# Optimization experiments

Hardware: AMD Instinct MI355X
Metric: run time of the kernel (lower is better)

Reference implementation:

```python
import jax, jax.numpy as jnp
import numpy as np

N_NODES = 20000
N_EDGES = 320000
HIDDEN = 64
HEADS = 8
HEAD_DIM = HIDDEN // HEADS
K_HOPS = 2
CST = 1e-05


def setup_inputs() -> dict:
    key = jax.random.key(0)
    ks = jax.random.split(key, 12)
    s = 1.0 / np.sqrt(HIDDEN)
    inp = {
        "x": jax.random.normal(ks[0], (N_NODES, HIDDEN), dtype=jnp.float32),
        "edge_index": jax.random.randint(ks[1], (2, N_EDGES), 0, N_NODES, dtype=jnp.int64),
        "edge_feature": jnp.zeros((1,), dtype=jnp.float32),  # unused by the module
        "Wq": jax.random.uniform(ks[2], (HIDDEN, HIDDEN), jnp.float32, -s, s),
        "bq": jax.random.uniform(ks[3], (HIDDEN,), jnp.float32, -s, s),
        "Wk": jax.random.uniform(ks[4], (HIDDEN, HIDDEN), jnp.float32, -s, s),
        "bk": jax.random.uniform(ks[5], (HIDDEN,), jnp.float32, -s, s),
        "Wv": jax.random.uniform(ks[6], (HIDDEN, HIDDEN), jnp.float32, -s, s),
        "bv": jax.random.uniform(ks[7], (HIDDEN,), jnp.float32, -s, s),
        "Wo": jax.random.uniform(ks[8], (HIDDEN, HIDDEN), jnp.float32, -s, s),
        "bo": jax.random.uniform(ks[9], (HIDDEN,), jnp.float32, -s, s),
        "hopwise": jnp.ones((K_HOPS + 1,), dtype=jnp.float32),
        "headwise": jnp.zeros((HEADS, K_HOPS), dtype=jnp.float32),
    }
    return inp


def reference(x, edge_index, edge_feature, Wq, bq, Wk, bk, Wv, bv, Wo, bo, hopwise, headwise):
    N = x.shape[0]
    row, col = edge_index[0], edge_index[1]

    # symmetric normalization: deg is in-degree of col
    deg = jax.ops.segment_sum(jnp.ones_like(col, dtype=x.dtype), col, num_segments=N)
    deg_inv = jnp.where(deg > 0, deg ** -0.5, 0.0)
    norm = deg_inv[row] * deg_inv[col]  # [E]

    Q = 1.0 + jax.nn.elu(x @ Wq + bq)
    K = 1.0 + jax.nn.elu(x @ Wk + bk)
    V = (x @ Wv + bv)
    Q = Q.reshape(N, HEADS, HEAD_DIM)
    K = K.reshape(N, HEADS, HEAD_DIM)
    V = V.reshape(N, HEADS, HEAD_DIM)

    M = jnp.einsum('nhi,nhj->nhij', K, V)  # [N,H,d,d]
    hidden = V * hopwise[0]
    layerwise = jax.nn.softmax(headwise, axis=0)  # softmax over heads (dim=-2)

    for hop in range(K_HOPS):
        # scatter-add propagation: out[i] = sum_{e: col[e]=i} norm[e] * state[row[e]]
        M = jax.ops.segment_sum(norm[:, None, None, None] * M[row], col, num_segments=N)
        K = jax.ops.segment_sum(norm[:, None, None] * K[row], col, num_segments=N)
        H = jnp.einsum('nhi,nhij->nhj', Q, M)
        C = jnp.einsum('nhi,nhi->nh', Q, K)[..., None] + CST
        H = H / C
        gamma = hopwise[hop + 1] * layerwise[:, hop][:, None]  # [H,1]
        hidden = hidden + gamma * H

    hidden = hidden.reshape(N, HEADS * HEAD_DIM)
    # dropout is identity in eval mode
    return hidden @ Wo + bo
```

## Files before the change

kernel.cpp:

```cpp
#include <hip/hip_runtime.h>
#include <hip/hip_bf16.h>

typedef __hip_bfloat16 bf16;
typedef __fp16 half2_t __attribute__((ext_vector_type(2)));
typedef float floatx2 __attribute__((ext_vector_type(2)));
typedef _Float16 f16x8_t __attribute__((ext_vector_type(8)));
typedef float f32x4_t __attribute__((ext_vector_type(4)));

#define N_NODES 20000
#define N_EDGES 320000
#define CSTF 1e-5f

#if defined(__has_builtin)
#if __has_builtin(__builtin_amdgcn_cvt_pk_fp8_f32) && __has_builtin(__builtin_amdgcn_cvt_pk_f32_fp8)
#define M1FP8 1
#endif
#if __has_builtin(__builtin_amdgcn_fdot2)
#define HAVE_FDOT2 1
#endif
#endif

#ifdef M1FP8
#define M1_STRIDE 128
#define M1_LANE   2
typedef uint2 m1vec;
#else
#define M1_STRIDE 256
#define M1_LANE   4
typedef uint4 m1vec;
#endif

__device__ __forceinline__ half2_t u2h(unsigned int u) {
    union { unsigned int u; half2_t h; } c; c.u = u; return c.h;
}
__device__ __forceinline__ unsigned int pkh(float a, float b) {
    union { __fp16 h[2]; unsigned int u; } c;
    c.h[0] = (__fp16)a; c.h[1] = (__fp16)b;
    return c.u;
}
__device__ __forceinline__ float fdot2(half2_t a, half2_t b, float c) {
#ifdef HAVE_FDOT2
    return __builtin_amdgcn_fdot2(a, b, c, false);
#else
    return fmaf((float)a.x, (float)b.x, fmaf((float)a.y, (float)b.y, c));
#endif
}
__device__ __forceinline__ int rdl(int v, int lane) { return __builtin_amdgcn_readlane(v, lane); }
__device__ __forceinline__ float ldf(const void* p, int i, bool bf) {
    return bf ? __bfloat162float(((const bf16*)p)[i]) : ((const float*)p)[i];
}
__device__ __forceinline__ bool wave_is_i64(const void* ei, int e) {
    unsigned int hi = ((const unsigned int*)ei)[2 * e + 1];
    return !__any(hi != 0);
}

struct Args {
    const void *x, *ei, *Wq, *bq, *Wk, *bk, *Wv, *bv, *Wo, *bo, *hopwise, *headwise;
    void* out;
    float* Q;
    _Float16 *K0h, *Vh, *K1h;
    unsigned int* M1h;
    int* bsrc;
    float* Hf;
    float* gam;
    int *deg, *cnt;
};

__global__ __launch_bounds__(256) void k_p1(Args a) {
    const int t = threadIdx.x;
    const int e = blockIdx.x * 256 + t;
    bool i64 = wave_is_i64(a.ei, e);
    int r, c;
    if (i64) {
        r = (int)((const long long*)a.ei)[e];
        c = (int)((const long long*)a.ei)[N_EDGES + e];
    } else {
        r = ((const int*)a.ei)[e];
        c = ((const int*)a.ei)[N_EDGES + e];
    }
    int slot = atomicAdd(&a.deg[c], 1);
    if (slot < 64) a.bsrc[c * 64 + slot] = r;
    if (blockIdx.x < 64) {
        int bad = 0;
        for (int i = blockIdx.x * 256 + t; i < 40000; i += 64 * 256) {
            unsigned int w = ((const unsigned int*)a.x)[i];
            if (((w >> 7)  & 0xFFu) == 0xFFu) bad++;
            if (((w >> 23) & 0xFFu) == 0xFFu) bad++;
        }
        if (bad) atomicAdd(&a.cnt[0], bad);
    }
}

__global__ __launch_bounds__(256) void k_qkv(Args a) {
    __shared__ __align__(16) _Float16 sA[4096];
    __shared__ __align__(16) _Float16 sB[12288];
    const int t = threadIdx.x;
    const bool bf = (a.cnt[0] < 16);
    const int n0 = blockIdx.x * 64;

    if (blockIdx.x == 0 && t < 8) {
        float e0 = 0.f, e1 = 0.f;
        for (int hh = 0; hh < 8; hh++) {
            e0 += __expf(ldf(a.headwise, hh * 2 + 0, bf));
            e1 += __expf(ldf(a.headwise, hh * 2 + 1, bf));
        }
        a.gam[t]     = ldf(a.hopwise, 1, bf) * __expf(ldf(a.headwise, t * 2 + 0, bf)) / e0;
        a.gam[8 + t] = ldf(a.hopwise, 2, bf) * __expf(ldf(a.headwise, t * 2 + 1, bf)) / e1;
        if (t == 0) a.gam[16] = ldf(a.hopwise, 0, bf);
    }

    for (int i = t; i < 2048; i += 256) {
        int node = i >> 5, kp = i & 31;
        int gn = n0 + node; if (gn >= N_NODES) gn = N_NODES - 1;
        float x0 = ldf(a.x, gn * 64 + kp * 2 + 0, bf);
        float x1 = ldf(a.x, gn * 64 + kp * 2 + 1, bf);
        int byte = (node * 128 + kp * 4) ^ ((node & 7) << 4);
        *(unsigned int*)((char*)sA + byte) = pkh(x0, x1);
    }
    for (int i = t; i < 6144; i += 256) {
        int kp = i / 192, n = i % 192;
        int k = kp * 2, c = n & 63;
        const void* W = (n < 64) ? a.Wq : (n < 128) ? a.Wk : a.Wv;
        float w0 = ldf(W, k * 64 + c, bf);
        float w1 = ldf(W, (k + 1) * 64 + c, bf);
        int ct = n >> 4, kh = k >> 5, kq = (k & 31) >> 3;
        int hoff = (((ct * 2 + kh) * 64 + kq * 16 + (n & 15)) << 3) + (k & 7);
        *(unsigned int*)&sB[hoff] = pkh(w0, w1);
    }
    __syncthreads();

    const int l = t & 63, w = t >> 6;
    f16x8_t Afrag[2];
    {
        int node = w * 16 + (l & 15);
        int cb = node * 128 + ((l >> 4) * 16);
        int swz = (node & 7) << 4;
        Afrag[0] = *(const f16x8_t*)((const char*)sA + ((cb)      ^ swz));
        Afrag[1] = *(const f16x8_t*)((const char*)sA + ((cb + 64) ^ swz));
    }
    f32x4_t acc[12];
#pragma unroll
    for (int ct = 0; ct < 12; ct++) acc[ct] = (f32x4_t){0.f, 0.f, 0.f, 0.f};
#pragma unroll
    for (int kh = 0; kh < 2; kh++) {
#pragma unroll
        for (int ct = 0; ct < 12; ct++) {
            f16x8_t B = *(const f16x8_t*)&sB[((ct * 2 + kh) * 64 + l) * 8];
            acc[ct] = __builtin_amdgcn_mfma_f32_16x16x32_f16(Afrag[kh], B, acc[ct], 0, 0, 0);
        }
    }
    const int dcol = l & 15;
    float bqv[4], bkv[4], bvv[4];
#pragma unroll
    for (int ct = 0; ct < 4; ct++) {
        bqv[ct] = ldf(a.bq, ct * 16 + dcol, bf);
        bkv[ct] = ldf(a.bk, ct * 16 + dcol, bf);
        bvv[ct] = ldf(a.bv, ct * 16 + dcol, bf);
    }
    const int rbase = n0 + w * 16 + ((l >> 4) << 2);
#pragma unroll
    for (int j = 0; j < 4; j++) {
        int gn = rbase + j;
        if (gn < N_NODES) {
            int dg = a.deg[gn];
            float di = dg > 0 ? rsqrtf((float)dg) : 0.0f;
#pragma unroll
            for (int ct = 0; ct < 4; ct++) {
                float q = acc[ct][j] + bqv[ct];
                a.Q[gn * 64 + ct * 16 + dcol] = q > 0.f ? q + 1.f : __expf(q);
                float kx = acc[4 + ct][j] + bkv[ct];
                float ke = kx > 0.f ? kx + 1.f : __expf(kx);
                a.K0h[gn * 64 + ct * 16 + dcol] = (_Float16)(di * ke);
                a.Vh[gn * 64 + ct * 16 + dcol] = (_Float16)(acc[8 + ct][j] + bvv[ct]);
            }
        }
    }
}

__global__ __launch_bounds__(128) void k_hop1(Args a) {
    const int l = threadIdx.x & 63;
    const int n = blockIdx.x * 2 + (threadIdx.x >> 6);
    const int hb = l & 56;
    float acc[8] = {0, 0, 0, 0, 0, 0, 0, 0};
    float kacc = 0.0f;
    const int dg = a.deg[n];
    const int m = min(dg, 64);
    if (m > 0) {
        const int srcv = a.bsrc[n * 64 + (l < m ? l : m - 1)];
#define H1_BODY(KU, VO, KO)                                                \
    {                                                                      \
        half2_t p0 = u2h(KU.x), p1 = u2h(KU.y), p2 = u2h(KU.z), p3 = u2h(KU.w); \
        float vv = (float)VO;                                              \
        acc[0] = fmaf(vv, (float)p0.x, acc[0]); acc[1] = fmaf(vv, (float)p0.y, acc[1]); \
        acc[2] = fmaf(vv, (float)p1.x, acc[2]); acc[3] = fmaf(vv, (float)p1.y, acc[3]); \
        acc[4] = fmaf(vv, (float)p2.x, acc[4]); acc[5] = fmaf(vv, (float)p2.y, acc[5]); \
        acc[6] = fmaf(vv, (float)p3.x, acc[6]); acc[7] = fmaf(vv, (float)p3.y, acc[7]); \
        kacc += (float)KO;                                                 \
    }
        int e = 0;
        for (; e + 4 <= m; e += 4) {
            int sA = rdl(srcv, e), sB = rdl(srcv, e + 1), sC = rdl(srcv, e + 2), sD = rdl(srcv, e + 3);
            uint4 kA = *(const uint4*)(a.K0h + sA * 64 + hb);
            uint4 kB = *(const uint4*)(a.K0h + sB * 64 + hb);
            uint4 kC = *(const uint4*)(a.K0h + sC * 64 + hb);
            uint4 kD = *(const uint4*)(a.K0h + sD * 64 + hb);
            __fp16 vA = a.Vh[sA * 64 + l], vB = a.Vh[sB * 64 + l];
            __fp16 vC = a.Vh[sC * 64 + l], vD = a.Vh[sD * 64 + l];
            __fp16 oA = a.K0h[sA * 64 + l], oB = a.K0h[sB * 64 + l];
            __fp16 oC = a.K0h[sC * 64 + l], oD = a.K0h[sD * 64 + l];
            H1_BODY(kA, vA, oA)
            H1_BODY(kB, vB, oB)
            H1_BODY(kC, vC, oC)
            H1_BODY(kD, vD, oD)
        }
        for (; e < m; e++) {
            int sA = rdl(srcv, e);
            uint4 kA = *(const uint4*)(a.K0h + sA * 64 + hb);
            __fp16 vA = a.Vh[sA * 64 + l];
            __fp16 oA = a.K0h[sA * 64 + l];
            H1_BODY(kA, vA, oA)
        }
#undef H1_BODY
        float inv = 1.0f / (float)dg;
#pragma unroll
        for (int i = 0; i < 8; i++) acc[i] *= inv;
        kacc *= inv;
    }
#ifdef M1FP8
    unsigned int w0 = 0, w1 = 0;
    w0 = __builtin_amdgcn_cvt_pk_fp8_f32(acc[0], acc[1], w0, false);
    w0 = __builtin_amdgcn_cvt_pk_fp8_f32(acc[2], acc[3], w0, true);
    w1 = __builtin_amdgcn_cvt_pk_fp8_f32(acc[4], acc[5], w1, false);
    w1 = __builtin_amdgcn_cvt_pk_fp8_f32(acc[6], acc[7], w1, true);
    uint2 o2; o2.x = w0; o2.y = w1;
    *(uint2*)(a.M1h + (size_t)n * M1_STRIDE + l * M1_LANE) = o2;
#else
    uint4 o;
    o.x = pkh(acc[0], acc[1]); o.y = pkh(acc[2], acc[3]);
    o.z = pkh(acc[4], acc[5]); o.w = pkh(acc[6], acc[7]);
    *(uint4*)(a.M1h + (size_t)n * M1_STRIDE + l * M1_LANE) = o;
#endif
    a.K1h[n * 64 + l] = (_Float16)kacc;
}

__global__ __launch_bounds__(128) void k_hop2f(Args a) {
    const int l = threadIdx.x & 63;
    const int n = blockIdx.x * 2 + (threadIdx.x >> 6);
    const int hb = l & 56, h = l >> 3;
    const float4 qa = *(const float4*)(a.Q + n * 64 + hb);
    const float4 qb = *(const float4*)(a.Q + n * 64 + hb + 4);
    const float qown = a.Q[n * 64 + l];
    float hacc = 0.0f, sk = 0.0f;
    const int dg = a.deg[n];
    const int m = min(dg, 64);
#ifdef M1FP8
#define H2_DOT(MU, DST)                                                    \
    {                                                                      \
        floatx2 a0 = __builtin_amdgcn_cvt_pk_f32_fp8(MU.x, false);         \
        floatx2 a1 = __builtin_amdgcn_cvt_pk_f32_fp8(MU.x, true);          \
        floatx2 a2 = __builtin_amdgcn_cvt_pk_f32_fp8(MU.y, false);         \
        floatx2 a3 = __builtin_amdgcn_cvt_pk_f32_fp8(MU.y, true);          \
        DST = qa.x * a0.x;                                                 \
        DST = fmaf(qa.y, a0.y, DST); DST = fmaf(qa.z, a1.x, DST);          \
        DST = fmaf(qa.w, a1.y, DST); DST = fmaf(qb.x, a2.x, DST);          \
        DST = fmaf(qb.y, a2.y, DST); DST = fmaf(qb.z, a3.x, DST);          \
        DST = fmaf(qb.w, a3.y, DST);                                       \
    }
#else
    const half2_t q01 = u2h(pkh(qa.x, qa.y));
    const half2_t q23 = u2h(pkh(qa.z, qa.w));
    const half2_t q45 = u2h(pkh(qb.x, qb.y));
    const half2_t q67 = u2h(pkh(qb.z, qb.w));
#define H2_DOT(MU, DST)                                                    \
    {                                                                      \
        DST = fdot2(q01, u2h(MU.x), 0.0f);                                 \
        DST = fdot2(q23, u2h(MU.y), DST);                                  \
        DST = fdot2(q45, u2h(MU.z), DST);                                  \
        DST = fdot2(q67, u2h(MU.w), DST);                                  \
    }
#endif
    if (m > 0) {
        const int srcv = a.bsrc[n * 64 + (l < m ? l : m - 1)];
        int e = 0;
        for (; e + 8 <= m; e += 8) {
            int s_[8];
            m1vec m_[8];
            __fp16 k_[8];
#pragma unroll
            for (int u = 0; u < 8; u++) s_[u] = rdl(srcv, e + u);
#pragma unroll
            for (int u = 0; u < 8; u++) m_[u] = *(const m1vec*)(a.M1h + (size_t)s_[u] * M1_STRIDE + l * M1_LANE);
#pragma unroll
            for (int u = 0; u < 8; u++) k_[u] = a.K1h[s_[u] * 64 + l];
#pragma unroll
            for (int u = 0; u < 8; u++) {
                float d;
                H2_DOT(m_[u], d)
                hacc += d;
                sk += (float)k_[u];
            }
        }
        for (; e < m; e++) {
            int sA = rdl(srcv, e);
            m1vec mA = *(const m1vec*)(a.M1h + (size_t)sA * M1_STRIDE + l * M1_LANE);
            __fp16 kA = a.K1h[sA * 64 + l];
            float d;
            H2_DOT(mA, d)
            hacc += d;
            sk += (float)kA;
        }
    }
    m1vec mo = *(const m1vec*)(a.M1h + (size_t)n * M1_STRIDE + l * M1_LANE);
    float h1r;
    H2_DOT(mo, h1r)
#undef H2_DOT
    const float din = dg > 0 ? rsqrtf((float)dg) : 0.0f;
    const float sq  = dg > 0 ? sqrtf((float)dg)  : 0.0f;
    float h1 = h1r * sq;
    float c1 = qown * (float)a.K1h[n * 64 + l];
    float c2 = qown * sk;
#pragma unroll
    for (int dd = 1; dd < 8; dd <<= 1) {
        c1 += __shfl_xor(c1, dd);
        c2 += __shfl_xor(c2, dd);
    }
    c1 *= sq;
    c2 *= din;
    float H2v = hacc * din;

    float hidden = a.gam[16] * (float)a.Vh[n * 64 + l]
                 + a.gam[h] * h1 / (c1 + CSTF)
                 + a.gam[8 + h] * H2v / (c2 + CSTF);
    a.Hf[n * 64 + l] = hidden;
}

__global__ __launch_bounds__(256) void k_out(Args a) {
    __shared__ __align__(16) _Float16 sA[4096];
    __shared__ __align__(16) _Float16 sB[4096];
    const int t = threadIdx.x;
    const bool bf = (a.cnt[0] < 16);
    const int n0 = blockIdx.x * 64;
    for (int i = t; i < 2048; i += 256) {
        int node = i >> 5, kp = i & 31;
        int gn = n0 + node; if (gn >= N_NODES) gn = N_NODES - 1;
        float2 hv = *(const float2*)(a.Hf + gn * 64 + kp * 2);
        int byte = (node * 128 + kp * 4) ^ ((node & 7) << 4);
        *(unsigned int*)((char*)sA + byte) = pkh(hv.x, hv.y);
    }
    for (int i = t; i < 2048; i += 256) {
        int kp = i >> 6, c = i & 63;
        int k = kp * 2;
        float w0 = ldf(a.Wo, k * 64 + c, bf);
        float w1 = ldf(a.Wo, (k + 1) * 64 + c, bf);
        int ct = c >> 4, kh = k >> 5, kq = (k & 31) >> 3;
        int hoff = (((ct * 2 + kh) * 64 + kq * 16 + (c & 15)) << 3) + (k & 7);
        *(unsigned int*)&sB[hoff] = pkh(w0, w1);
    }
    __syncthreads();
    const int l = t & 63, w = t >> 6;
    f16x8_t Afrag[2];
    {
        int node = w * 16 + (l & 15);
        int cb = node * 128 + ((l >> 4) * 16);
        int swz = (node & 7) << 4;
        Afrag[0] = *(const f16x8_t*)((const char*)sA + ((cb)      ^ swz));
        Afrag[1] = *(const f16x8_t*)((const char*)sA + ((cb + 64) ^ swz));
    }
    f32x4_t acc[4];
#pragma unroll
    for (int ct = 0; ct < 4; ct++) acc[ct] = (f32x4_t){0.f, 0.f, 0.f, 0.f};
#pragma unroll
    for (int kh = 0; kh < 2; kh++) {
#pragma unroll
        for (int ct = 0; ct < 4; ct++) {
            f16x8_t B = *(const f16x8_t*)&sB[((ct * 2 + kh) * 64 + l) * 8];
            acc[ct] = __builtin_amdgcn_mfma_f32_16x16x32_f16(Afrag[kh], B, acc[ct], 0, 0, 0);
        }
    }
    const int dcol = l & 15;
    float bov[4];
#pragma unroll
    for (int ct = 0; ct < 4; ct++) bov[ct] = ldf(a.bo, ct * 16 + dcol, bf);
    const int rbase = n0 + w * 16 + ((l >> 4) << 2);
#pragma unroll
    for (int j = 0; j < 4; j++) {
        int gn = rbase + j;
        if (gn < N_NODES) {
#pragma unroll
            for (int ct = 0; ct < 4; ct++) {
                float o = acc[ct][j] + bov[ct];
                if (bf) ((bf16*)a.out)[gn * 64 + ct * 16 + dcol] = __float2bfloat16(o);
                else    ((float*)a.out)[gn * 64 + ct * 16 + dcol] = o;
            }
        }
    }
}

extern "C" void kernel_launch(void* const* d_in, const int* in_sizes, int n_in,
                              void* d_out, int out_size, void* d_ws, size_t ws_size,
                              hipStream_t stream) {
    char* p = (char*)d_ws;
    auto alloc = [&](size_t bytes) {
        void* r = (void*)p;
        p += (bytes + 255) & ~(size_t)255;
        return r;
    };
    Args a;
    a.x = d_in[0];  a.ei = d_in[1];
    a.Wq = d_in[3]; a.bq = d_in[4];
    a.Wk = d_in[5]; a.bk = d_in[6];
    a.Wv = d_in[7]; a.bv = d_in[8];
    a.Wo = d_in[9]; a.bo = d_in[10];
    a.hopwise = d_in[11]; a.headwise = d_in[12];
    a.out = d_out;

    a.Q    = (float*)alloc((size_t)N_NODES * 64 * 4);
    a.K0h  = (_Float16*)alloc((size_t)N_NODES * 64 * 2);
    a.Vh   = (_Float16*)alloc((size_t)N_NODES * 64 * 2);
    a.K1h  = (_Float16*)alloc((size_t)N_NODES * 64 * 2);
    a.M1h  = (unsigned int*)alloc((size_t)N_NODES * 1024);
    a.Hf   = (float*)alloc((size_t)N_NODES * 64 * 4);
    a.bsrc = (int*)alloc((size_t)N_NODES * 64 * 4);
    a.gam  = (float*)alloc(256);
    int* zz = (int*)alloc(((size_t)N_NODES + 64) * 4);
    a.deg = zz;
    a.cnt = zz + N_NODES;

    (void)hipMemsetAsync(zz, 0, ((size_t)N_NODES + 64) * 4, stream);

    const int EB = (N_EDGES + 255) / 256;
    const int GB = (N_NODES + 63) / 64;
    k_p1<<<EB, 256, 0, stream>>>(a);
    k_qkv<<<GB, 256, 0, stream>>>(a);
    k_hop1<<<N_NODES / 2, 128, 0, stream>>>(a);
    k_hop2f<<<N_NODES / 2, 128, 0, stream>>>(a);
    k_out<<<GB, 256, 0, stream>>>(a);
}
```

Baseline: 173.8 us.

## Fuse hop-2 aggregation with output projection and vectorize x loads

Merges the second-hop aggregation kernel with the output linear layer. Each 512-thread block handles 8 nodes, stages their hidden vectors as fp16 in shared memory, and runs the Wo projection with MFMA directly, so the fp32 Hf intermediate buffer and one kernel launch go away. Each block now re-stages the full Wo matrix into shared memory, and four of its eight waves sit idle during the small MFMA, which wastes half of each 16-row tile. Separately, the x staging in the QKV kernel now reads packed pairs with a single wider load instead of two scalar loads.

```diff
diff --git a/kernel.cpp b/kernel.cpp
--- a/kernel.cpp
+++ b/kernel.cpp
@@ -49,6 +49,9 @@
 __device__ __forceinline__ float ldf(const void* p, int i, bool bf) {
     return bf ? __bfloat162float(((const bf16*)p)[i]) : ((const float*)p)[i];
 }
+__device__ __forceinline__ float bfbits(unsigned int lo16) {
+    union { unsigned int u; float f; } c; c.u = lo16 << 16; return c.f;
+}
 __device__ __forceinline__ bool wave_is_i64(const void* ei, int e) {
     unsigned int hi = ((const unsigned int*)ei)[2 * e + 1];
     return !__any(hi != 0);
@@ -61,7 +64,6 @@
     _Float16 *K0h, *Vh, *K1h;
     unsigned int* M1h;
     int* bsrc;
-    float* Hf;
     float* gam;
     int *deg, *cnt;
 };
@@ -112,8 +114,14 @@
     for (int i = t; i < 2048; i += 256) {
         int node = i >> 5, kp = i & 31;
         int gn = n0 + node; if (gn >= N_NODES) gn = N_NODES - 1;
-        float x0 = ldf(a.x, gn * 64 + kp * 2 + 0, bf);
-        float x1 = ldf(a.x, gn * 64 + kp * 2 + 1, bf);
+        float x0, x1;
+        if (bf) {
+            unsigned int u = ((const unsigned int*)a.x)[gn * 32 + kp];
+            x0 = bfbits(u & 0xFFFFu); x1 = bfbits(u >> 16);
+        } else {
+            float2 xv = ((const float2*)a.x)[gn * 32 + kp];
+            x0 = xv.x; x1 = xv.y;
+        }
         int byte = (node * 128 + kp * 4) ^ ((node & 7) << 4);
         *(unsigned int*)((char*)sA + byte) = pkh(x0, x1);
     }
@@ -243,10 +251,26 @@
     a.K1h[n * 64 + l] = (_Float16)kacc;
 }
 
-__global__ __launch_bounds__(128) void k_hop2f(Args a) {
-    const int l = threadIdx.x & 63;
-    const int n = blockIdx.x * 2 + (threadIdx.x >> 6);
+__global__ __launch_bounds__(512, 4) void k_hop2o(Args a) {
+    __shared__ __align__(16) _Float16 sH[1024];
+    __shared__ __align__(16) _Float16 sWo[4096];
+    const int t = threadIdx.x;
+    const bool bf = (a.cnt[0] < 16);
+    const int l = t & 63;
+    const int wv = t >> 6;
+    const int n = blockIdx.x * 8 + wv;
     const int hb = l & 56, h = l >> 3;
+
+    for (int i = t; i < 2048; i += 512) {
+        int kp = i >> 6, c = i & 63;
+        int k = kp * 2;
+        float w0 = ldf(a.Wo, k * 64 + c, bf);
+        float w1 = ldf(a.Wo, (k + 1) * 64 + c, bf);
+        int ct = c >> 4, kh = k >> 5, kq = (k & 31) >> 3;
+        int hoff = (((ct * 2 + kh) * 64 + kq * 16 + (c & 15)) << 3) + (k & 7);
+        *(unsigned int*)&sWo[hoff] = pkh(w0, w1);
+    }
+
     const float4 qa = *(const float4*)(a.Q + n * 64 + hb);
     const float4 qb = *(const float4*)(a.Q + n * 64 + hb + 4);
     const float qown = a.Q[n * 64 + l];
@@ -331,66 +355,35 @@
     float hidden = a.gam[16] * (float)a.Vh[n * 64 + l]
                  + a.gam[h] * h1 / (c1 + CSTF)
                  + a.gam[8 + h] * H2v / (c2 + CSTF);
-    a.Hf[n * 64 + l] = hidden;
-}
-
-__global__ __launch_bounds__(256) void k_out(Args a) {
-    __shared__ __align__(16) _Float16 sA[4096];
-    __shared__ __align__(16) _Float16 sB[4096];
-    const int t = threadIdx.x;
-    const bool bf = (a.cnt[0] < 16);
-    const int n0 = blockIdx.x * 64;
-    for (int i = t; i < 2048; i += 256) {
-        int node = i >> 5, kp = i & 31;
-        int gn = n0 + node; if (gn >= N_NODES) gn = N_NODES - 1;
-        float2 hv = *(const float2*)(a.Hf + gn * 64 + kp * 2);
-        int byte = (node * 128 + kp * 4) ^ ((node & 7) << 4);
-        *(unsigned int*)((char*)sA + byte) = pkh(hv.x, hv.y);
-    }
-    for (int i = t; i < 2048; i += 256) {
-        int kp = i >> 6, c = i & 63;
-        int k = kp * 2;
-        float w0 = ldf(a.Wo, k * 64 + c, bf);
-        float w1 = ldf(a.Wo, (k + 1) * 64 + c, bf);
-        int ct = c >> 4, kh = k >> 5, kq = (k & 31) >> 3;
-        int hoff = (((ct * 2 + kh) * 64 + kq * 16 + (c & 15)) << 3) + (k & 7);
-        *(unsigned int*)&sB[hoff] = pkh(w0, w1);
+
+    {
+        int byte = (wv * 128 + l * 2) ^ ((wv & 7) << 4);
+        *(_Float16*)((char*)sH + byte) = (_Float16)hidden;
     }
     __syncthreads();
-    const int l = t & 63, w = t >> 6;
-    f16x8_t Afrag[2];
-    {
-        int node = w * 16 + (l & 15);
-        int cb = node * 128 + ((l >> 4) * 16);
-        int swz = (node & 7) << 4;
-        Afrag[0] = *(const f16x8_t*)((const char*)sA + ((cb)      ^ swz));
-        Afrag[1] = *(const f16x8_t*)((const char*)sA + ((cb + 64) ^ swz));
-    }
-    f32x4_t acc[4];
-#pragma unroll
-    for (int ct = 0; ct < 4; ct++) acc[ct] = (f32x4_t){0.f, 0.f, 0.f, 0.f};
-#pragma unroll
-    for (int kh = 0; kh < 2; kh++) {
-#pragma unroll
-        for (int ct = 0; ct < 4; ct++) {
-            f16x8_t B = *(const f16x8_t*)&sB[((ct * 2 + kh) * 64 + l) * 8];
-            acc[ct] = __builtin_amdgcn_mfma_f32_16x16x32_f16(Afrag[kh], B, acc[ct], 0, 0, 0);
-        }
-    }
-    const int dcol = l & 15;
-    float bov[4];
-#pragma unroll
-    for (int ct = 0; ct < 4; ct++) bov[ct] = ldf(a.bo, ct * 16 + dcol, bf);
-    const int rbase = n0 + w * 16 + ((l >> 4) << 2);
-#pragma unroll
-    for (int j = 0; j < 4; j++) {
-        int gn = rbase + j;
-        if (gn < N_NODES) {
-#pragma unroll
-            for (int ct = 0; ct < 4; ct++) {
-                float o = acc[ct][j] + bov[ct];
-                if (bf) ((bf16*)a.out)[gn * 64 + ct * 16 + dcol] = __float2bfloat16(o);
-                else    ((float*)a.out)[gn * 64 + ct * 16 + dcol] = o;
+
+    if (wv < 4) {
+        const int ct = wv;
+        int row = l & 15;
+        int swz = (row & 7) << 4;
+        int cb = row * 128 + ((l >> 4) * 16);
+        f16x8_t A0 = *(const f16x8_t*)((const char*)sH + ((cb)      ^ swz));
+        f16x8_t A1 = *(const f16x8_t*)((const char*)sH + ((cb + 64) ^ swz));
+        f32x4_t acc = (f32x4_t){0.f, 0.f, 0.f, 0.f};
+        f16x8_t B0 = *(const f16x8_t*)&sWo[((ct * 2 + 0) * 64 + l) * 8];
+        f16x8_t B1 = *(const f16x8_t*)&sWo[((ct * 2 + 1) * 64 + l) * 8];
+        acc = __builtin_amdgcn_mfma_f32_16x16x32_f16(A0, B0, acc, 0, 0, 0);
+        acc = __builtin_amdgcn_mfma_f32_16x16x32_f16(A1, B1, acc, 0, 0, 0);
+        const int dcol = l & 15;
+        const float bov = ldf(a.bo, ct * 16 + dcol, bf);
+        const int rb = (l >> 4) * 4;
+        if (rb < 8) {
+            const int gb = blockIdx.x * 8 + rb;
+#pragma unroll
+            for (int j = 0; j < 4; j++) {
+                float o = acc[j] + bov;
+                if (bf) ((bf16*)a.out)[(gb + j) * 64 + ct * 16 + dcol] = __float2bfloat16(o);
+                else    ((float*)a.out)[(gb + j) * 64 + ct * 16 + dcol] = o;
             }
         }
     }
@@ -419,7 +412,6 @@
     a.Vh   = (_Float16*)alloc((size_t)N_NODES * 64 * 2);
     a.K1h  = (_Float16*)alloc((size_t)N_NODES * 64 * 2);
     a.M1h  = (unsigned int*)alloc((size_t)N_NODES * 1024);
-    a.Hf   = (float*)alloc((size_t)N_NODES * 64 * 4);
     a.bsrc = (int*)alloc((size_t)N_NODES * 64 * 4);
     a.gam  = (float*)alloc(256);
     int* zz = (int*)alloc(((size_t)N_NODES + 64) * 4);
@@ -433,6 +425,5 @@
     k_p1<<<EB, 256, 0, stream>>>(a);
     k_qkv<<<GB, 256, 0, stream>>>(a);
     k_hop1<<<N_NODES / 2, 128, 0, stream>>>(a);
-    k_hop2f<<<N_NODES / 2, 128, 0, stream>>>(a);
-    k_out<<<GB, 256, 0, stream>>>(a);
-}
+    k_hop2o<<<N_NODES / 8, 512, 0, stream>>>(a);
+}
```

Measured after the change: 174.2 us. No clear change (+0.3%).
